# Optimization experiments

Measured on AMD Instinct MI355X. Metric: run time of the kernel, lower is better.

The kernel has to match this reference:

```python
import jax, jax.numpy as jnp
import numpy as np

N_NODES = 100000
N_EDGES = 1600000
N_IN = 256
N_H = 128


def setup_inputs() -> dict:
    key = jax.random.key(0)
    k1, k2, k3, k4 = jax.random.split(key, 4)
    x = jax.random.normal(k1, (N_NODES, N_IN), dtype=jnp.float32)
    edge_index = jax.random.randint(k2, (2, N_EDGES), 0, N_NODES, dtype=jnp.int64)
    # GCNConv weights (glorot-like scale) and biases
    W1 = jax.random.normal(k3, (N_IN, N_H), dtype=jnp.float32) / np.sqrt(N_IN)
    b1 = jnp.zeros((N_H,), dtype=jnp.float32)
    W2 = jax.random.normal(k4, (N_H, N_H), dtype=jnp.float32) / np.sqrt(N_H)
    b2 = jnp.zeros((N_H,), dtype=jnp.float32)
    return {"x": x, "W1": W1, "b1": b1, "W2": W2, "b2": b2, "edge_index": edge_index}


def _gcn_conv(x, W, b, row, col, n_nodes):
    """PyG GCNConv: add self-loops, symmetric norm D^-1/2 A D^-1/2, aggregate at target (col)."""
    h = x @ W  # [N, out]
    # degree including self-loop (edge_weight = 1): deg[i] = 1 + #incoming edges at target i
    deg = jnp.ones((n_nodes,), dtype=x.dtype).at[col].add(1.0)
    dinv = jax.lax.rsqrt(deg)
    # off-diagonal edges: msg j->i weighted by dinv[j]*dinv[i]
    norm = dinv[row] * dinv[col]  # [E]
    msg = h[row] * norm[:, None]  # [E, out]
    agg = jax.ops.segment_sum(msg, col, num_segments=n_nodes)
    # self-loop contribution: weight dinv[i]^2
    agg = agg + h * (dinv * dinv)[:, None]
    return agg + b


def reference(x, W1, b1, W2, b2, edge_index):
    row, col = edge_index[0], edge_index[1]
    n = x.shape[0]
    out = jax.nn.relu(_gcn_conv(x, W1, b1, row, col, n))
    out = _gcn_conv(out, W2, b2, row, col, n)
    return out
```

## Files before the change

kernel.cpp:

```cpp
#include <hip/hip_runtime.h>


#define NN 100000
#define NH 128
#define NB 196
#define SB 256

__device__ __forceinline__ float bf2f(unsigned int u) { return __uint_as_float(u << 16); }
__device__ __forceinline__ unsigned short f2bf(float f) {
    unsigned int u = __float_as_uint(f);
    u = (u + 0x7fffu + ((u >> 16) & 1u)) >> 16;
    return (unsigned short)u;
}

__device__ __forceinline__ void dma16(const void* g, void* l) {
    __builtin_amdgcn_global_load_lds(
        (const __attribute__((address_space(1))) unsigned int*)g,
        (__attribute__((address_space(3))) unsigned int*)l, 16, 0, 0);
}

__global__ __launch_bounds__(256) void k_hist(const int* __restrict__ col,
                                              int* __restrict__ blockCnt, int E, int chb) {
    __shared__ int h[NB];
    int t = threadIdx.x, blk = blockIdx.x;
    if (t < NB) h[t] = 0;
    __syncthreads();
    int s = blk * chb, en = min(E, s + chb);
    for (int e = s + t; e < en; e += 256) atomicAdd(&h[col[e] >> 9], 1);
    __syncthreads();
    if (t < NB) blockCnt[t * SB + blk] = h[t];
}

__global__ __launch_bounds__(256) void k_base(const int* __restrict__ blockCnt,
                                              int* __restrict__ base) {
    __shared__ int s[256];
    int t = threadIdx.x;
    int tot = 0;
    if (t < NB)
        for (int j = 0; j < SB; ++j) tot += blockCnt[t * SB + j];
    s[t] = tot;
    __syncthreads();
    for (int off = 1; off < 256; off <<= 1) {
        int v = (t >= off) ? s[t - off] : 0;
        __syncthreads();
        s[t] += v;
        __syncthreads();
    }
    if (t < NB) base[t] = s[t] - tot;
    if (t == NB - 1) base[NB] = s[t];
}

__global__ __launch_bounds__(256) void k_bscan(const int* __restrict__ blockCnt,
                                               const int* __restrict__ base,
                                               int* __restrict__ blockOff) {
    __shared__ int s[256];
    int t = threadIdx.x, b = blockIdx.x;
    int v = blockCnt[b * SB + t];
    s[t] = v;
    __syncthreads();
    for (int off = 1; off < 256; off <<= 1) {
        int u = (t >= off) ? s[t - off] : 0;
        __syncthreads();
        s[t] += u;
        __syncthreads();
    }
    blockOff[b * SB + t] = base[b] + s[t] - v;
}

__global__ __launch_bounds__(256) void k_scatter(const int* __restrict__ row,
                                                 const int* __restrict__ col,
                                                 const int* __restrict__ blockOff,
                                                 unsigned int* __restrict__ pairs,
                                                 int E, int chb) {
    __shared__ int cur[NB];
    __shared__ int bof[NB];
    int t = threadIdx.x, blk = blockIdx.x;
    if (t < NB) {
        cur[t] = 0;
        bof[t] = blockOff[t * SB + blk];
    }
    __syncthreads();
    int s = blk * chb, en = min(E, s + chb);
    for (int e = s + t; e < en; e += 256) {
        int c = col[e];
        int b = c >> 9;
        int r = atomicAdd(&cur[b], 1);
        pairs[bof[b] + r] = (unsigned int)row[e] | ((unsigned int)(c & 511) << 17);
    }
}

__global__ __launch_bounds__(512) void k_bin(const unsigned int* __restrict__ pairs,
                                             const int* __restrict__ base,
                                             unsigned int* __restrict__ csr,
                                             int* __restrict__ offs,
                                             float* __restrict__ dinv, int n) {
    __shared__ int cnt[512];
    __shared__ int s[512];
    int t = threadIdx.x, b = blockIdx.x;
    cnt[t] = 0;
    __syncthreads();
    int e0 = base[b], e1 = base[b + 1];
    for (int i = e0 + t; i < e1; i += 512) atomicAdd(&cnt[pairs[i] >> 17], 1);
    __syncthreads();
    int v = cnt[t];
    int node = b * 512 + t;
    if (node < n) dinv[node] = rsqrtf(1.0f + (float)v);
    s[t] = v;
    __syncthreads();
    for (int off = 1; off < 512; off <<= 1) {
        int u = (t >= off) ? s[t - off] : 0;
        __syncthreads();
        s[t] += u;
        __syncthreads();
    }
    int excl = s[t] - v;
    if (node <= n) offs[node] = e0 + excl;
    __syncthreads();
    cnt[t] = e0 + excl;
    __syncthreads();
    for (int i = e0 + t; i < e1; i += 512) {
        unsigned int p = pairs[i];
        int d = atomicAdd(&cnt[p >> 17], 1);
        csr[d] = p & 0x1FFFFu;
    }
}

__global__ void k_wprep(const float* __restrict__ W, unsigned short* __restrict__ Thi,
                        unsigned short* __restrict__ Tlo, int K) {
    int idx = blockIdx.x * 256 + threadIdx.x;
    if (idx >= K * 128) return;
    int k = idx >> 7, c = idx & 127;
    float w = W[idx];
    unsigned int u = __float_as_uint(w) & 0xffff0000u;
    float rem = w - __uint_as_float(u);
    Thi[(size_t)c * K + k] = (unsigned short)(u >> 16);
    Tlo[(size_t)c * K + k] = (unsigned short)(__float_as_uint(rem) >> 16);
}

template <int K>
__global__ __launch_bounds__(256) void k_gemm_mfma(const float* __restrict__ A,
                                                   const unsigned short* __restrict__ Bhi,
                                                   const unsigned short* __restrict__ Blo,
                                                   const float* __restrict__ dinv,
                                                   unsigned short* __restrict__ C, int M) {
    using bf16x8 = __attribute__((ext_vector_type(8))) short;
    using f32x4  = __attribute__((ext_vector_type(4))) float;
    constexpr int T = K / 32;
    __shared__ uint4 sA4[2][1024];
    __shared__ uint4 sB4[2][2][512];

    const int lane = threadIdx.x & 63;
    const int wv   = threadIdx.x >> 6;
    const int r    = lane & 15;
    const int kb   = lane >> 4;
    const int rowBase = blockIdx.x * 128;

    auto stage = [&](int ks, int b) {
        const int kk = ks * 32;
#pragma unroll
        for (int c = 0; c < 4; ++c) {
            int sb = wv * 256 + c * 64;
            int s  = sb + lane;
            int akb = s >> 8, aj = (s >> 7) & 1, ar = s & 127;
            int gr = rowBase + ar; if (gr >= M) gr = M - 1;
            dma16(A + (size_t)gr * K + kk + akb * 8 + aj * 4, &sA4[b][sb]);
        }
#pragma unroll
        for (int hl = 0; hl < 2; ++hl) {
            const unsigned short* Bp = hl ? Blo : Bhi;
#pragma unroll
            for (int c = 0; c < 2; ++c) {
                int sb = wv * 128 + c * 64;
                int s  = sb + lane;
                int bkb = s >> 7, bcol = s & 127;
                dma16(Bp + (size_t)bcol * K + kk + bkb * 8, &sB4[b][hl][sb]);
            }
        }
    };

    f32x4 acc[2][8];
#pragma unroll
    for (int m = 0; m < 2; ++m)
#pragma unroll
        for (int t = 0; t < 8; ++t) acc[m][t] = (f32x4){0.f, 0.f, 0.f, 0.f};

    stage(0, 0);
    __syncthreads();
#pragma unroll
    for (int ks = 0; ks < T; ++ks) {
        const int buf = ks & 1;
        if (ks + 1 < T) stage(ks + 1, buf ^ 1);
        bf16x8 ah[2], al[2];
#pragma unroll
        for (int m = 0; m < 2; ++m) {
            int rowl = wv * 32 + m * 16 + r;
            uint4 u0 = sA4[buf][kb * 256 + rowl];
            uint4 u1 = sA4[buf][kb * 256 + 128 + rowl];
            float f[8];
            *(uint4*)&f[0] = u0;
            *(uint4*)&f[4] = u1;
#pragma unroll
            for (int j = 0; j < 8; ++j) {
                float x = f[j];
                unsigned int u = __float_as_uint(x) & 0xffff0000u;
                ah[m][j] = (short)(u >> 16);
                al[m][j] = (short)(__float_as_uint(x - __uint_as_float(u)) >> 16);
            }
        }
#pragma unroll
        for (int t = 0; t < 8; ++t) {
            int col = t * 16 + r;
            bf16x8 bh = *(const bf16x8*)&sB4[buf][0][kb * 128 + col];
            bf16x8 bl = *(const bf16x8*)&sB4[buf][1][kb * 128 + col];
#pragma unroll
            for (int m = 0; m < 2; ++m) {
                acc[m][t] = __builtin_amdgcn_mfma_f32_16x16x32_bf16(ah[m], bh, acc[m][t], 0, 0, 0);
                acc[m][t] = __builtin_amdgcn_mfma_f32_16x16x32_bf16(al[m], bh, acc[m][t], 0, 0, 0);
                acc[m][t] = __builtin_amdgcn_mfma_f32_16x16x32_bf16(ah[m], bl, acc[m][t], 0, 0, 0);
            }
        }
        __syncthreads();
    }
    const int wrow = rowBase + wv * 32;
#pragma unroll
    for (int m = 0; m < 2; ++m) {
#pragma unroll
        for (int q = 0; q < 4; ++q) {
            int orow = wrow + m * 16 + kb * 4 + q;
            if (orow < M) {
                float dv = dinv[orow];
#pragma unroll
                for (int t = 0; t < 8; ++t)
                    C[(size_t)orow * 128 + t * 16 + r] = f2bf(acc[m][t][q] * dv);
            }
        }
    }
}

template <int K>
__global__ __launch_bounds__(256) void k_gemm_bf16(const unsigned short* __restrict__ A,
                                                   const unsigned short* __restrict__ Bhi,
                                                   const unsigned short* __restrict__ Blo,
                                                   const float* __restrict__ dinv,
                                                   unsigned short* __restrict__ C, int M) {
    using bf16x8 = __attribute__((ext_vector_type(8))) short;
    using f32x4  = __attribute__((ext_vector_type(4))) float;
    constexpr int T = K / 32;
    __shared__ uint4 sA2[2][512];
    __shared__ uint4 sB4[2][2][512];

    const int lane = threadIdx.x & 63;
    const int wv   = threadIdx.x >> 6;
    const int r    = lane & 15;
    const int kb   = lane >> 4;
    const int rowBase = blockIdx.x * 128;

    auto stage = [&](int ks, int b) {
        const int kk = ks * 32;
#pragma unroll
        for (int c = 0; c < 2; ++c) {
            int sb = wv * 128 + c * 64;
            int s  = sb + lane;
            int akb = s >> 7, ar = s & 127;
            int gr = rowBase + ar; if (gr >= M) gr = M - 1;
            dma16(A + (size_t)gr * K + kk + akb * 8, &sA2[b][sb]);
        }
#pragma unroll
        for (int hl = 0; hl < 2; ++hl) {
            const unsigned short* Bp = hl ? Blo : Bhi;
#pragma unroll
            for (int c = 0; c < 2; ++c) {
                int sb = wv * 128 + c * 64;
                int s  = sb + lane;
                int bkb = s >> 7, bcol = s & 127;
                dma16(Bp + (size_t)bcol * K + kk + bkb * 8, &sB4[b][hl][sb]);
            }
        }
    };

    f32x4 acc[2][8];
#pragma unroll
    for (int m = 0; m < 2; ++m)
#pragma unroll
        for (int t = 0; t < 8; ++t) acc[m][t] = (f32x4){0.f, 0.f, 0.f, 0.f};

    stage(0, 0);
    __syncthreads();
#pragma unroll
    for (int ks = 0; ks < T; ++ks) {
        const int buf = ks & 1;
        if (ks + 1 < T) stage(ks + 1, buf ^ 1);
#pragma unroll
        for (int t = 0; t < 8; ++t) {
            int col = t * 16 + r;
            bf16x8 bh = *(const bf16x8*)&sB4[buf][0][kb * 128 + col];
            bf16x8 bl = *(const bf16x8*)&sB4[buf][1][kb * 128 + col];
#pragma unroll
            for (int m = 0; m < 2; ++m) {
                bf16x8 a = *(const bf16x8*)&sA2[buf][kb * 128 + wv * 32 + m * 16 + r];
                acc[m][t] = __builtin_amdgcn_mfma_f32_16x16x32_bf16(a, bh, acc[m][t], 0, 0, 0);
                acc[m][t] = __builtin_amdgcn_mfma_f32_16x16x32_bf16(a, bl, acc[m][t], 0, 0, 0);
            }
        }
        __syncthreads();
    }
    const int wrow = rowBase + wv * 32;
#pragma unroll
    for (int m = 0; m < 2; ++m) {
#pragma unroll
        for (int q = 0; q < 4; ++q) {
            int orow = wrow + m * 16 + kb * 4 + q;
            if (orow < M) {
                float dv = dinv[orow];
#pragma unroll
                for (int t = 0; t < 8; ++t)
                    C[(size_t)orow * 128 + t * 16 + r] = f2bf(acc[m][t][q] * dv);
            }
        }
    }
}

#define ACC8(u)                                              \
    a[0] += bf2f(u.x & 0xffffu); a[1] += bf2f(u.x >> 16);    \
    a[2] += bf2f(u.y & 0xffffu); a[3] += bf2f(u.y >> 16);    \
    a[4] += bf2f(u.z & 0xffffu); a[5] += bf2f(u.z >> 16);    \
    a[6] += bf2f(u.w & 0xffffu); a[7] += bf2f(u.w >> 16);

template <bool RELU, bool BF16OUT>
__global__ __launch_bounds__(256) void k_agg(const unsigned short* __restrict__ hb,
                                             const float* __restrict__ dinv,
                                             const int* __restrict__ off,
                                             const unsigned int* __restrict__ csr,
                                             const float* __restrict__ bias,
                                             void* __restrict__ outv, int n) {
    int gid  = blockIdx.x * 256 + threadIdx.x;
    int node = gid >> 4;
    int lane = gid & 15;
    if (node >= n) return;
    float di = dinv[node];
    uint4 us = *(const uint4*)(hb + ((size_t)node << 7) + lane * 8);
    float a[8];
    a[0] = bf2f(us.x & 0xffffu); a[1] = bf2f(us.x >> 16);
    a[2] = bf2f(us.y & 0xffffu); a[3] = bf2f(us.y >> 16);
    a[4] = bf2f(us.z & 0xffffu); a[5] = bf2f(us.z >> 16);
    a[6] = bf2f(us.w & 0xffffu); a[7] = bf2f(us.w >> 16);
    int e  = off[node];
    int e1 = off[node + 1];
    for (; e + 8 <= e1; e += 8) {
        unsigned int s0 = csr[e + 0], s1 = csr[e + 1], s2 = csr[e + 2], s3 = csr[e + 3];
        unsigned int s4 = csr[e + 4], s5 = csr[e + 5], s6 = csr[e + 6], s7 = csr[e + 7];
        uint4 u0 = *(const uint4*)(hb + ((size_t)s0 << 7) + lane * 8);
        uint4 u1 = *(const uint4*)(hb + ((size_t)s1 << 7) + lane * 8);
        uint4 u2 = *(const uint4*)(hb + ((size_t)s2 << 7) + lane * 8);
        uint4 u3 = *(const uint4*)(hb + ((size_t)s3 << 7) + lane * 8);
        uint4 u4 = *(const uint4*)(hb + ((size_t)s4 << 7) + lane * 8);
        uint4 u5 = *(const uint4*)(hb + ((size_t)s5 << 7) + lane * 8);
        uint4 u6 = *(const uint4*)(hb + ((size_t)s6 << 7) + lane * 8);
        uint4 u7 = *(const uint4*)(hb + ((size_t)s7 << 7) + lane * 8);
        ACC8(u0) ACC8(u1) ACC8(u2) ACC8(u3) ACC8(u4) ACC8(u5) ACC8(u6) ACC8(u7)
    }
    for (; e + 4 <= e1; e += 4) {
        unsigned int s0 = csr[e + 0], s1 = csr[e + 1], s2 = csr[e + 2], s3 = csr[e + 3];
        uint4 u0 = *(const uint4*)(hb + ((size_t)s0 << 7) + lane * 8);
        uint4 u1 = *(const uint4*)(hb + ((size_t)s1 << 7) + lane * 8);
        uint4 u2 = *(const uint4*)(hb + ((size_t)s2 << 7) + lane * 8);
        uint4 u3 = *(const uint4*)(hb + ((size_t)s3 << 7) + lane * 8);
        ACC8(u0) ACC8(u1) ACC8(u2) ACC8(u3)
    }
    for (; e < e1; ++e) {
        unsigned int s = csr[e];
        uint4 u = *(const uint4*)(hb + ((size_t)s << 7) + lane * 8);
        ACC8(u)
    }
    float4 b0 = *(const float4*)&bias[lane * 8];
    float4 b1 = *(const float4*)&bias[lane * 8 + 4];
    a[0] = a[0] * di + b0.x; a[1] = a[1] * di + b0.y;
    a[2] = a[2] * di + b0.z; a[3] = a[3] * di + b0.w;
    a[4] = a[4] * di + b1.x; a[5] = a[5] * di + b1.y;
    a[6] = a[6] * di + b1.z; a[7] = a[7] * di + b1.w;
    if (RELU) {
#pragma unroll
        for (int j = 0; j < 8; ++j) a[j] = fmaxf(a[j], 0.f);
    }
    if (BF16OUT) {
        uint4 o;
        o.x = (unsigned int)f2bf(a[0]) | ((unsigned int)f2bf(a[1]) << 16);
        o.y = (unsigned int)f2bf(a[2]) | ((unsigned int)f2bf(a[3]) << 16);
        o.z = (unsigned int)f2bf(a[4]) | ((unsigned int)f2bf(a[5]) << 16);
        o.w = (unsigned int)f2bf(a[6]) | ((unsigned int)f2bf(a[7]) << 16);
        *(uint4*)((unsigned short*)outv + ((size_t)node << 7) + lane * 8) = o;
    } else {
        float* op = (float*)outv + ((size_t)node << 7) + lane * 8;
        *(float4*)op       = make_float4(a[0], a[1], a[2], a[3]);
        *(float4*)(op + 4) = make_float4(a[4], a[5], a[6], a[7]);
    }
}

extern "C" void kernel_launch(void* const* d_in, const int* in_sizes, int n_in,
                              void* d_out, int out_size, void* d_ws, size_t ws_size,
                              hipStream_t stream) {
    const float* x  = (const float*)d_in[0];
    const float* W1 = (const float*)d_in[1];
    const float* b1 = (const float*)d_in[2];
    const float* W2 = (const float*)d_in[3];
    const float* b2 = (const float*)d_in[4];
    const int*   ei = (const int*)d_in[5];

    const int n = NN;
    const int E = in_sizes[5] / 2;
    const int* row = ei;
    const int* col = ei + E;

    char* ws = (char*)d_ws;
    size_t o = 0;
    auto alloc = [&](size_t bytes) {
        void* p = ws + o;
        o = (o + bytes + 255) & ~(size_t)255;
        return p;
    };
    int*            blockCnt = (int*)alloc((size_t)NB * SB * 4);
    int*            blockOff = (int*)alloc((size_t)NB * SB * 4);
    int*            base     = (int*)alloc((size_t)(NB + 1) * 4);
    int*            offs     = (int*)alloc((size_t)(n + 1) * 4);
    float*          dinv     = (float*)alloc((size_t)n * 4);
    unsigned int*   pairs    = (unsigned int*)alloc((size_t)E * 4);
    unsigned int*   csr      = (unsigned int*)alloc((size_t)E * 4);
    unsigned short* bufH     = (unsigned short*)alloc((size_t)n * NH * 2);
    unsigned short* bufG     = (unsigned short*)alloc((size_t)n * NH * 2);
    unsigned short* wt1hi    = (unsigned short*)alloc(256 * 128 * 2);
    unsigned short* wt1lo    = (unsigned short*)alloc(256 * 128 * 2);
    unsigned short* wt2hi    = (unsigned short*)alloc(128 * 128 * 2);
    unsigned short* wt2lo    = (unsigned short*)alloc(128 * 128 * 2);

    const int chb = (E + SB - 1) / SB;

    k_wprep<<<(256 * 128 + 255) / 256, 256, 0, stream>>>(W1, wt1hi, wt1lo, 256);
    k_wprep<<<(128 * 128 + 255) / 256, 256, 0, stream>>>(W2, wt2hi, wt2lo, 128);

    k_hist<<<SB, 256, 0, stream>>>(col, blockCnt, E, chb);
    k_base<<<1, 256, 0, stream>>>(blockCnt, base);
    k_bscan<<<NB, 256, 0, stream>>>(blockCnt, base, blockOff);
    k_scatter<<<SB, 256, 0, stream>>>(row, col, blockOff, pairs, E, chb);
    k_bin<<<NB, 512, 0, stream>>>(pairs, base, csr, offs, dinv, n);

    int aggBlocks = (n + 15) / 16;
    int gemmBlocks = (n + 127) / 128;
    k_gemm_mfma<256><<<gemmBlocks, 256, 0, stream>>>(x, wt1hi, wt1lo, dinv, bufH, n);
    k_agg<true, true><<<aggBlocks, 256, 0, stream>>>(bufH, dinv, offs, csr, b1, bufG, n);
    k_gemm_bf16<128><<<gemmBlocks, 256, 0, stream>>>(bufG, wt2hi, wt2lo, dinv, bufH, n);
    k_agg<false, false><<<aggBlocks, 256, 0, stream>>>(bufH, dinv, offs, csr, b2, d_out, n);
}
```

Before: 255.0 us.

## Drop split-bf16 emulation in GEMMs and use XOR-swizzled LDS layouts

Both GEMMs stop emulating fp32 with hi/lo bf16 splits (three or two MFMAs per tile) and instead do a single bf16 MFMA with round-to-nearest conversion of A and W. The LDS staging layouts are reorganized into row-major tiles with XOR swizzles to avoid bank conflicts, and weight prep produces a single bf16 copy. This cuts MFMA work and LDS/global traffic for the weights, at the cost of lower GEMM accuracy that could approach tolerance limits.

```diff
diff --git a/kernel.cpp b/kernel.cpp
--- a/kernel.cpp
+++ b/kernel.cpp
@@ -125,29 +125,23 @@
     }
 }
 
-__global__ void k_wprep(const float* __restrict__ W, unsigned short* __restrict__ Thi,
-                        unsigned short* __restrict__ Tlo, int K) {
+__global__ void k_wprep(const float* __restrict__ W, unsigned short* __restrict__ T, int K) {
     int idx = blockIdx.x * 256 + threadIdx.x;
     if (idx >= K * 128) return;
     int k = idx >> 7, c = idx & 127;
-    float w = W[idx];
-    unsigned int u = __float_as_uint(w) & 0xffff0000u;
-    float rem = w - __uint_as_float(u);
-    Thi[(size_t)c * K + k] = (unsigned short)(u >> 16);
-    Tlo[(size_t)c * K + k] = (unsigned short)(__float_as_uint(rem) >> 16);
+    T[(size_t)c * K + k] = f2bf(W[idx]);
 }
 
 template <int K>
 __global__ __launch_bounds__(256) void k_gemm_mfma(const float* __restrict__ A,
-                                                   const unsigned short* __restrict__ Bhi,
-                                                   const unsigned short* __restrict__ Blo,
+                                                   const unsigned short* __restrict__ Bt,
                                                    const float* __restrict__ dinv,
                                                    unsigned short* __restrict__ C, int M) {
     using bf16x8 = __attribute__((ext_vector_type(8))) short;
     using f32x4  = __attribute__((ext_vector_type(4))) float;
     constexpr int T = K / 32;
-    __shared__ uint4 sA4[2][1024];
-    __shared__ uint4 sB4[2][2][512];
+    __shared__ uint4 sA[2][1024];
+    __shared__ uint4 sB[2][512];
 
     const int lane = threadIdx.x & 63;
     const int wv   = threadIdx.x >> 6;
@@ -160,21 +154,17 @@
 #pragma unroll
         for (int c = 0; c < 4; ++c) {
             int sb = wv * 256 + c * 64;
-            int s  = sb + lane;
-            int akb = s >> 8, aj = (s >> 7) & 1, ar = s & 127;
-            int gr = rowBase + ar; if (gr >= M) gr = M - 1;
-            dma16(A + (size_t)gr * K + kk + akb * 8 + aj * 4, &sA4[b][sb]);
-        }
-#pragma unroll
-        for (int hl = 0; hl < 2; ++hl) {
-            const unsigned short* Bp = hl ? Blo : Bhi;
-#pragma unroll
-            for (int c = 0; c < 2; ++c) {
-                int sb = wv * 128 + c * 64;
-                int s  = sb + lane;
-                int bkb = s >> 7, bcol = s & 127;
-                dma16(Bp + (size_t)bcol * K + kk + bkb * 8, &sB4[b][hl][sb]);
-            }
+            int q  = sb + lane;
+            int row = q >> 3, pg = (q & 7) ^ (row & 7);
+            int gr = rowBase + row; if (gr >= M) gr = M - 1;
+            dma16(A + (size_t)gr * K + kk + pg * 4, &sA[b][sb]);
+        }
+#pragma unroll
+        for (int c = 0; c < 2; ++c) {
+            int sb = wv * 128 + c * 64;
+            int q  = sb + lane;
+            int bc = q >> 2, pg = (q & 3) ^ (bc & 3);
+            dma16(Bt + (size_t)bc * K + kk + pg * 8, &sB[b][sb]);
         }
     };
 
@@ -190,34 +180,27 @@
     for (int ks = 0; ks < T; ++ks) {
         const int buf = ks & 1;
         if (ks + 1 < T) stage(ks + 1, buf ^ 1);
-        bf16x8 ah[2], al[2];
+        bf16x8 ah[2];
 #pragma unroll
         for (int m = 0; m < 2; ++m) {
             int rowl = wv * 32 + m * 16 + r;
-            uint4 u0 = sA4[buf][kb * 256 + rowl];
-            uint4 u1 = sA4[buf][kb * 256 + 128 + rowl];
+            int p0 = (2 * kb)     ^ (rowl & 7);
+            int p1 = (2 * kb + 1) ^ (rowl & 7);
+            uint4 u0 = sA[buf][rowl * 8 + p0];
+            uint4 u1 = sA[buf][rowl * 8 + p1];
             float f[8];
             *(uint4*)&f[0] = u0;
             *(uint4*)&f[4] = u1;
 #pragma unroll
-            for (int j = 0; j < 8; ++j) {
-                float x = f[j];
-                unsigned int u = __float_as_uint(x) & 0xffff0000u;
-                ah[m][j] = (short)(u >> 16);
-                al[m][j] = (short)(__float_as_uint(x - __uint_as_float(u)) >> 16);
-            }
+            for (int j = 0; j < 8; ++j) ah[m][j] = (short)f2bf(f[j]);
         }
 #pragma unroll
         for (int t = 0; t < 8; ++t) {
-            int col = t * 16 + r;
-            bf16x8 bh = *(const bf16x8*)&sB4[buf][0][kb * 128 + col];
-            bf16x8 bl = *(const bf16x8*)&sB4[buf][1][kb * 128 + col];
-#pragma unroll
-            for (int m = 0; m < 2; ++m) {
+            int bc = t * 16 + r;
+            bf16x8 bh = *(const bf16x8*)&sB[buf][bc * 4 + (kb ^ (bc & 3))];
+#pragma unroll
+            for (int m = 0; m < 2; ++m)
                 acc[m][t] = __builtin_amdgcn_mfma_f32_16x16x32_bf16(ah[m], bh, acc[m][t], 0, 0, 0);
-                acc[m][t] = __builtin_amdgcn_mfma_f32_16x16x32_bf16(al[m], bh, acc[m][t], 0, 0, 0);
-                acc[m][t] = __builtin_amdgcn_mfma_f32_16x16x32_bf16(ah[m], bl, acc[m][t], 0, 0, 0);
-            }
         }
         __syncthreads();
     }
@@ -239,15 +222,14 @@
 
 template <int K>
 __global__ __launch_bounds__(256) void k_gemm_bf16(const unsigned short* __restrict__ A,
-                                                   const unsigned short* __restrict__ Bhi,
-                                                   const unsigned short* __restrict__ Blo,
+                                                   const unsigned short* __restrict__ Bt,
                                                    const float* __restrict__ dinv,
                                                    unsigned short* __restrict__ C, int M) {
     using bf16x8 = __attribute__((ext_vector_type(8))) short;
     using f32x4  = __attribute__((ext_vector_type(4))) float;
     constexpr int T = K / 32;
-    __shared__ uint4 sA2[2][512];
-    __shared__ uint4 sB4[2][2][512];
+    __shared__ uint4 sA[2][512];
+    __shared__ uint4 sB[2][512];
 
     const int lane = threadIdx.x & 63;
     const int wv   = threadIdx.x >> 6;
@@ -260,21 +242,17 @@
 #pragma unroll
         for (int c = 0; c < 2; ++c) {
             int sb = wv * 128 + c * 64;
-            int s  = sb + lane;
-            int akb = s >> 7, ar = s & 127;
-            int gr = rowBase + ar; if (gr >= M) gr = M - 1;
-            dma16(A + (size_t)gr * K + kk + akb * 8, &sA2[b][sb]);
-        }
-#pragma unroll
-        for (int hl = 0; hl < 2; ++hl) {
-            const unsigned short* Bp = hl ? Blo : Bhi;
-#pragma unroll
-            for (int c = 0; c < 2; ++c) {
-                int sb = wv * 128 + c * 64;
-                int s  = sb + lane;
-                int bkb = s >> 7, bcol = s & 127;
-                dma16(Bp + (size_t)bcol * K + kk + bkb * 8, &sB4[b][hl][sb]);
-            }
+            int q  = sb + lane;
+            int row = q >> 2, pg = (q & 3) ^ (row & 3);
+            int gr = rowBase + row; if (gr >= M) gr = M - 1;
+            dma16(A + (size_t)gr * K + kk + pg * 8, &sA[b][sb]);
+        }
+#pragma unroll
+        for (int c = 0; c < 2; ++c) {
+            int sb = wv * 128 + c * 64;
+            int q  = sb + lane;
+            int bc = q >> 2, pg = (q & 3) ^ (bc & 3);
+            dma16(Bt + (size_t)bc * K + kk + pg * 8, &sB[b][sb]);
         }
     };
 
@@ -290,17 +268,19 @@
     for (int ks = 0; ks < T; ++ks) {
         const int buf = ks & 1;
         if (ks + 1 < T) stage(ks + 1, buf ^ 1);
+        bf16x8 a[2];
+#pragma unroll
+        for (int m = 0; m < 2; ++m) {
+            int rowl = wv * 32 + m * 16 + r;
+            a[m] = *(const bf16x8*)&sA[buf][rowl * 4 + (kb ^ (rowl & 3))];
+        }
 #pragma unroll
         for (int t = 0; t < 8; ++t) {
-            int col = t * 16 + r;
-            bf16x8 bh = *(const bf16x8*)&sB4[buf][0][kb * 128 + col];
-            bf16x8 bl = *(const bf16x8*)&sB4[buf][1][kb * 128 + col];
-#pragma unroll
-            for (int m = 0; m < 2; ++m) {
-                bf16x8 a = *(const bf16x8*)&sA2[buf][kb * 128 + wv * 32 + m * 16 + r];
-                acc[m][t] = __builtin_amdgcn_mfma_f32_16x16x32_bf16(a, bh, acc[m][t], 0, 0, 0);
-                acc[m][t] = __builtin_amdgcn_mfma_f32_16x16x32_bf16(a, bl, acc[m][t], 0, 0, 0);
-            }
+            int bc = t * 16 + r;
+            bf16x8 bh = *(const bf16x8*)&sB[buf][bc * 4 + (kb ^ (bc & 3))];
+#pragma unroll
+            for (int m = 0; m < 2; ++m)
+                acc[m][t] = __builtin_amdgcn_mfma_f32_16x16x32_bf16(a[m], bh, acc[m][t], 0, 0, 0);
         }
         __syncthreads();
     }
@@ -427,15 +407,13 @@
     unsigned int*   csr      = (unsigned int*)alloc((size_t)E * 4);
     unsigned short* bufH     = (unsigned short*)alloc((size_t)n * NH * 2);
     unsigned short* bufG     = (unsigned short*)alloc((size_t)n * NH * 2);
-    unsigned short* wt1hi    = (unsigned short*)alloc(256 * 128 * 2);
-    unsigned short* wt1lo    = (unsigned short*)alloc(256 * 128 * 2);
-    unsigned short* wt2hi    = (unsigned short*)alloc(128 * 128 * 2);
-    unsigned short* wt2lo    = (unsigned short*)alloc(128 * 128 * 2);
+    unsigned short* wt1      = (unsigned short*)alloc(256 * 128 * 2);
+    unsigned short* wt2      = (unsigned short*)alloc(128 * 128 * 2);
 
     const int chb = (E + SB - 1) / SB;
 
-    k_wprep<<<(256 * 128 + 255) / 256, 256, 0, stream>>>(W1, wt1hi, wt1lo, 256);
-    k_wprep<<<(128 * 128 + 255) / 256, 256, 0, stream>>>(W2, wt2hi, wt2lo, 128);
+    k_wprep<<<(256 * 128 + 255) / 256, 256, 0, stream>>>(W1, wt1, 256);
+    k_wprep<<<(128 * 128 + 255) / 256, 256, 0, stream>>>(W2, wt2, 128);
 
     k_hist<<<SB, 256, 0, stream>>>(col, blockCnt, E, chb);
     k_base<<<1, 256, 0, stream>>>(blockCnt, base);
@@ -445,8 +423,8 @@
 
     int aggBlocks = (n + 15) / 16;
     int gemmBlocks = (n + 127) / 128;
-    k_gemm_mfma<256><<<gemmBlocks, 256, 0, stream>>>(x, wt1hi, wt1lo, dinv, bufH, n);
+    k_gemm_mfma<256><<<gemmBlocks, 256, 0, stream>>>(x, wt1, dinv, bufH, n);
     k_agg<true, true><<<aggBlocks, 256, 0, stream>>>(bufH, dinv, offs, csr, b1, bufG, n);
-    k_gemm_bf16<128><<<gemmBlocks, 256, 0, stream>>>(bufG, wt2hi, wt2lo, dinv, bufH, n);
+    k_gemm_bf16<128><<<gemmBlocks, 256, 0, stream>>>(bufG, wt2, dinv, bufH, n);
     k_agg<false, false><<<aggBlocks, 256, 0, stream>>>(bufH, dinv, offs, csr, b2, d_out, n);
 }
```

Result: faster. 227.8 us (-10.6%).
